# Kernel tuning notes

Hardware: AMD Instinct MI355X
Metric: run time of the kernel (lower is better)

## Reference

```python
import jax, jax.numpy as jnp
import numpy as np

D_IN = 1024
D_OUT = 1024
NUM_HEADS = 16
HEAD_DIM = D_OUT // NUM_HEADS


def setup_inputs() -> dict:
    key = jax.random.key(0)
    ks = jax.random.split(key, 6)
    scale = 0.02
    x = jax.random.normal(ks[0], (4, 2048, D_IN), dtype=jnp.float32)
    Wq = jax.random.normal(ks[1], (D_IN, D_OUT), dtype=jnp.float32) * scale
    Wk = jax.random.normal(ks[2], (D_IN, D_OUT), dtype=jnp.float32) * scale
    Wv = jax.random.normal(ks[3], (D_IN, D_OUT), dtype=jnp.float32) * scale
    Wo = jax.random.normal(ks[4], (D_OUT, D_OUT), dtype=jnp.float32) * scale
    bo = jax.random.normal(ks[5], (D_OUT,), dtype=jnp.float32) * scale
    return {"x": x, "Wq": Wq, "Wk": Wk, "Wv": Wv, "Wo": Wo, "bo": bo}


def reference(x, Wq, Wk, Wv, Wo, bo):
    b, n, _ = x.shape
    # QKV projections -> [b, h, n, hd]
    def split_heads(t):
        return t.reshape(b, n, NUM_HEADS, HEAD_DIM).transpose(0, 2, 1, 3)
    q = split_heads(x @ Wq)
    k = split_heads(x @ Wk)
    v = split_heads(x @ Wv)
    # scaled causal attention scores [b, h, n, n]
    scores = jnp.einsum('bhqd,bhkd->bhqk', q, k) / jnp.sqrt(jnp.float32(HEAD_DIM))
    causal = jnp.tril(jnp.ones((n, n), dtype=bool))
    scores = jnp.where(causal, scores, -jnp.inf)
    attn = jax.nn.softmax(scores, axis=-1)
    # dropout p=0.0 -> identity
    ctx = jnp.einsum('bhqk,bhkd->bhqd', attn, v)  # [b, h, n, hd]
    ctx = ctx.transpose(0, 2, 1, 3).reshape(b, n, D_OUT)
    return ctx @ Wo + bo
```

## Files before the change

### kernel.cpp

```cpp
#include <hip/hip_runtime.h>
#include <hip/hip_bf16.h>

typedef __bf16 bf16;
typedef __attribute__((ext_vector_type(8))) __bf16 bf16x8;
typedef __attribute__((ext_vector_type(4))) __bf16 bf16x4;
typedef __attribute__((ext_vector_type(4))) float floatx4;

#define DM 1024
#define NH 16
#define HD 64
#define SEQ 2048
#define BATCH 4
#define MTOT (BATCH * SEQ)

#define GLDS(g, l) \
  __builtin_amdgcn_global_load_lds((const __attribute__((address_space(1))) void*)(g), \
                                   (__attribute__((address_space(3))) void*)(l), 16, 0, 0)

__global__ void cvt_f32_bf16(const float* __restrict__ in, bf16* __restrict__ out, int n4) {
  int i = blockIdx.x * 256 + threadIdx.x;
  if (i < n4) {
    float4 v = ((const float4*)in)[i];
    bf16x4 o;
    o[0] = (bf16)v.x; o[1] = (bf16)v.y; o[2] = (bf16)v.z; o[3] = (bf16)v.w;
    ((bf16x4*)out)[i] = o;
  }
}

__global__ void transpose_cvt4(const float* __restrict__ Wq, const float* __restrict__ Wk,
                               const float* __restrict__ Wv, const float* __restrict__ Wo,
                               bf16* __restrict__ Wqkvt, bf16* __restrict__ Wot) {
  __shared__ float tile[32][33];
  const float* W;
  bf16* Wt;
  int z = blockIdx.z;
  if (z == 0) { W = Wq; Wt = Wqkvt; }
  else if (z == 1) { W = Wk; Wt = Wqkvt + (size_t)DM * DM; }
  else if (z == 2) { W = Wv; Wt = Wqkvt + (size_t)2 * DM * DM; }
  else { W = Wo; Wt = Wot; }
  int n0 = blockIdx.x * 32, k0 = blockIdx.y * 32;
  int tx = threadIdx.x, ty = threadIdx.y;
#pragma unroll
  for (int j = 0; j < 32; j += 8)
    tile[ty + j][tx] = W[(size_t)(k0 + ty + j) * DM + n0 + tx];
  __syncthreads();
#pragma unroll
  for (int j = 0; j < 32; j += 8)
    Wt[(size_t)(n0 + ty + j) * DM + k0 + tx] = (bf16)tile[tx][ty + j];
}

#define BK 64

__global__ __launch_bounds__(256, 3) void gemm_qkv(const bf16* __restrict__ A,
                                                   const bf16* __restrict__ Bt,
                                                   bf16* __restrict__ Qb,
                                                   bf16* __restrict__ Kb,
                                                   bf16* __restrict__ Vt) {
  __shared__ __align__(16) bf16 Alds[128 * BK];
  __shared__ __align__(16) bf16 Blds[128 * BK];
  const int K = 1024;
  int m0 = blockIdx.x * 128;
  int n0 = blockIdx.y * 128;
  int tid = threadIdx.x;
  int wave = tid >> 6, lane = tid & 63;
  int wm = (wave & 1) * 64, wn = (wave >> 1) * 64;
  int lm = lane & 15, quad = lane >> 4;
  int lm7 = lm & 7;

  int cbase = wave * 64 + lane;
  const bf16* gA[4];
  const bf16* gB[4];
  bf16 *lA[4], *lB[4];
#pragma unroll
  for (int seg = 0; seg < 4; ++seg) {
    int c = seg * 256 + cbase;
    int row = c >> 3;
    int col8 = (c & 7) ^ (row & 7);
    gA[seg] = A + (size_t)(m0 + row) * K + col8 * 8;
    gB[seg] = Bt + (size_t)(n0 + row) * K + col8 * 8;
    lA[seg] = Alds + c * 8;
    lB[seg] = Blds + c * 8;
  }

  floatx4 acc[4][4] = {};
  for (int kt = 0; kt < K; kt += BK) {
    __syncthreads();
#pragma unroll
    for (int seg = 0; seg < 4; ++seg) {
      GLDS(gA[seg] + kt, lA[seg]);
      GLDS(gB[seg] + kt, lB[seg]);
    }
    __syncthreads();
#pragma unroll
    for (int ks = 0; ks < 2; ++ks) {
      int xk = (ks * 4 + quad) ^ lm7;
      bf16x8 af[4], bfr[4];
#pragma unroll
      for (int t = 0; t < 4; ++t) {
        af[t] = *(const bf16x8*)(Alds + (wm + t * 16 + lm) * BK + xk * 8);
        bfr[t] = *(const bf16x8*)(Blds + (wn + t * 16 + lm) * BK + xk * 8);
      }
#pragma unroll
      for (int i = 0; i < 4; ++i)
#pragma unroll
        for (int j = 0; j < 4; ++j)
          acc[i][j] = __builtin_amdgcn_mfma_f32_16x16x32_bf16(af[i], bfr[j], acc[i][j], 0, 0, 0);
    }
  }
#pragma unroll
  for (int i = 0; i < 4; ++i) {
#pragma unroll
    for (int j = 0; j < 4; ++j) {
#pragma unroll
      for (int r = 0; r < 4; ++r) {
        int R = m0 + wm + i * 16 + quad * 4 + r;
        int C = n0 + wn + j * 16 + lm;
        int b = R >> 11, n = R & 2047;
        int proj = C >> 10, c = C & 1023;
        int h = c >> 6, d = c & 63;
        int bh = b * NH + h;
        bf16 bv = (bf16)acc[i][j][r];
        if (proj == 0)
          Qb[((size_t)bh * SEQ + n) * HD + d] = bv;
        else if (proj == 1)
          Kb[((size_t)bh * SEQ + n) * HD + d] = bv;
        else
          Vt[((size_t)bh * HD + d) * SEQ + n] = bv;
      }
    }
  }
}

__global__ __launch_bounds__(256, 3) void gemm_out(const bf16* __restrict__ A,
                                                   const bf16* __restrict__ Bt,
                                                   const float* __restrict__ bias,
                                                   float* __restrict__ out) {
  __shared__ __align__(16) bf16 Alds[128 * BK];
  __shared__ __align__(16) bf16 Blds[128 * BK];
  const int K = 1024;
  int m0 = blockIdx.x * 128;
  int n0 = blockIdx.y * 128;
  int tid = threadIdx.x;
  int wave = tid >> 6, lane = tid & 63;
  int wm = (wave & 1) * 64, wn = (wave >> 1) * 64;
  int lm = lane & 15, quad = lane >> 4;
  int lm7 = lm & 7;

  int cbase = wave * 64 + lane;
  const bf16* gA[4];
  const bf16* gB[4];
  bf16 *lA[4], *lB[4];
#pragma unroll
  for (int seg = 0; seg < 4; ++seg) {
    int c = seg * 256 + cbase;
    int row = c >> 3;
    int col8 = (c & 7) ^ (row & 7);
    gA[seg] = A + (size_t)(m0 + row) * K + col8 * 8;
    gB[seg] = Bt + (size_t)(n0 + row) * K + col8 * 8;
    lA[seg] = Alds + c * 8;
    lB[seg] = Blds + c * 8;
  }

  floatx4 acc[4][4] = {};
  for (int kt = 0; kt < K; kt += BK) {
    __syncthreads();
#pragma unroll
    for (int seg = 0; seg < 4; ++seg) {
      GLDS(gA[seg] + kt, lA[seg]);
      GLDS(gB[seg] + kt, lB[seg]);
    }
    __syncthreads();
#pragma unroll
    for (int ks = 0; ks < 2; ++ks) {
      int xk = (ks * 4 + quad) ^ lm7;
      bf16x8 af[4], bfr[4];
#pragma unroll
      for (int t = 0; t < 4; ++t) {
        af[t] = *(const bf16x8*)(Alds + (wm + t * 16 + lm) * BK + xk * 8);
        bfr[t] = *(const bf16x8*)(Blds + (wn + t * 16 + lm) * BK + xk * 8);
      }
#pragma unroll
      for (int i = 0; i < 4; ++i)
#pragma unroll
        for (int j = 0; j < 4; ++j)
          acc[i][j] = __builtin_amdgcn_mfma_f32_16x16x32_bf16(af[i], bfr[j], acc[i][j], 0, 0, 0);
    }
  }
#pragma unroll
  for (int i = 0; i < 4; ++i)
#pragma unroll
    for (int j = 0; j < 4; ++j)
#pragma unroll
      for (int r = 0; r < 4; ++r) {
        int R = m0 + wm + i * 16 + quad * 4 + r;
        int C = n0 + wn + j * 16 + lm;
        out[(size_t)R * DM + C] = acc[i][j][r] + bias[C];
      }
}

#define SKV 72

__global__ __launch_bounds__(256) void attn(const bf16* __restrict__ Qb,
                                            const bf16* __restrict__ Kb,
                                            const bf16* __restrict__ Vt,
                                            bf16* __restrict__ ctx) {
  __shared__ __align__(16) bf16 Klds[64 * SKV];
  __shared__ __align__(16) bf16 Vlds[64 * SKV];
  __shared__ __align__(16) bf16 Plds[4 * 16 * SKV];
  int blk = blockIdx.x;
  int xcd = blk & 7;
  int k = blk >> 3;
  int p = k & 15;
  int bh = (k >> 4) * 8 + xcd;
  int tid = threadIdx.x, wave = tid >> 6, lane = tid & 63;
  int lm = lane & 15, quad = lane >> 4;
  const bf16* Qp = Qb + (size_t)bh * SEQ * HD;
  const bf16* Kp = Kb + (size_t)bh * SEQ * HD;
  const bf16* Vp = Vt + (size_t)bh * HD * SEQ;
  bf16* Pl = Plds + wave * 16 * SKV;
  int sr = tid >> 3, sc = (tid & 7) * 8;
  int b = bh >> 4, h = bh & 15;

#pragma unroll 1
  for (int phase = 0; phase < 2; ++phase) {
    int qt = phase ? (31 - p) : p;
    int q0 = qt * 64;
    int rowbase = q0 + wave * 16;

    bf16x8 qf[2];
#pragma unroll
    for (int ks = 0; ks < 2; ++ks) {
      bf16x8 q = *(const bf16x8*)(Qp + (size_t)(rowbase + lm) * HD + ks * 32 + quad * 8);
#pragma unroll
      for (int j = 0; j < 8; ++j) q[j] = (bf16)((float)q[j] * 0.125f);
      qf[ks] = q;
    }

    floatx4 acco[4] = {};
    float lsum[4] = {};
    int nkv = qt + 1;

    bf16x8 ka0 = *(const bf16x8*)(Kp + (size_t)sr * HD + sc);
    bf16x8 ka1 = *(const bf16x8*)(Kp + (size_t)(32 + sr) * HD + sc);
    bf16x8 va0 = *(const bf16x8*)(Vp + (size_t)sr * SEQ + sc);
    bf16x8 va1 = *(const bf16x8*)(Vp + (size_t)(32 + sr) * SEQ + sc);
    __syncthreads();
    *(bf16x8*)(Klds + sr * SKV + sc) = ka0;
    *(bf16x8*)(Klds + (32 + sr) * SKV + sc) = ka1;
    *(bf16x8*)(Vlds + sr * SKV + sc) = va0;
    *(bf16x8*)(Vlds + (32 + sr) * SKV + sc) = va1;

#pragma unroll 1
    for (int t = 0; t < nkv; ++t) {
      __syncthreads();
      int kv0 = t * 64;
      if (t + 1 < nkv) {
        int kn = kv0 + 64;
        ka0 = *(const bf16x8*)(Kp + (size_t)(kn + sr) * HD + sc);
        ka1 = *(const bf16x8*)(Kp + (size_t)(kn + 32 + sr) * HD + sc);
        va0 = *(const bf16x8*)(Vp + (size_t)sr * SEQ + kn + sc);
        va1 = *(const bf16x8*)(Vp + (size_t)(32 + sr) * SEQ + kn + sc);
      }

      floatx4 s[4] = {};
#pragma unroll
      for (int nt = 0; nt < 4; ++nt) {
        bf16x8 kf0 = *(const bf16x8*)(Klds + (nt * 16 + lm) * SKV + quad * 8);
        bf16x8 kf1 = *(const bf16x8*)(Klds + (nt * 16 + lm) * SKV + 32 + quad * 8);
        s[nt] = __builtin_amdgcn_mfma_f32_16x16x32_bf16(qf[0], kf0, s[nt], 0, 0, 0);
        s[nt] = __builtin_amdgcn_mfma_f32_16x16x32_bf16(qf[1], kf1, s[nt], 0, 0, 0);
      }

      if (t != qt) {
#pragma unroll
        for (int nt = 0; nt < 4; ++nt)
#pragma unroll
          for (int r = 0; r < 4; ++r) {
            float pv = __expf(s[nt][r]);
            lsum[r] += pv;
            Pl[(quad * 4 + r) * SKV + nt * 16 + lm] = (bf16)pv;
          }
      } else {
#pragma unroll
        for (int nt = 0; nt < 4; ++nt)
#pragma unroll
          for (int r = 0; r < 4; ++r) {
            int rowrel = wave * 16 + quad * 4 + r;
            float pv = __expf(s[nt][r]);
            if (nt * 16 + lm > rowrel) pv = 0.f;
            lsum[r] += pv;
            Pl[(quad * 4 + r) * SKV + nt * 16 + lm] = (bf16)pv;
          }
      }

#pragma unroll
      for (int ks = 0; ks < 2; ++ks) {
        bf16x8 pf = *(const bf16x8*)(Pl + lm * SKV + ks * 32 + quad * 8);
#pragma unroll
        for (int db = 0; db < 4; ++db) {
          bf16x8 vf = *(const bf16x8*)(Vlds + (db * 16 + lm) * SKV + ks * 32 + quad * 8);
          acco[db] = __builtin_amdgcn_mfma_f32_16x16x32_bf16(pf, vf, acco[db], 0, 0, 0);
        }
      }

      if (t + 1 < nkv) {
        __syncthreads();
        *(bf16x8*)(Klds + sr * SKV + sc) = ka0;
        *(bf16x8*)(Klds + (32 + sr) * SKV + sc) = ka1;
        *(bf16x8*)(Vlds + sr * SKV + sc) = va0;
        *(bf16x8*)(Vlds + (32 + sr) * SKV + sc) = va1;
      }
    }

#pragma unroll
    for (int r = 0; r < 4; ++r) {
      float l = lsum[r];
      l += __shfl_xor(l, 1, 64);
      l += __shfl_xor(l, 2, 64);
      l += __shfl_xor(l, 4, 64);
      l += __shfl_xor(l, 8, 64);
      lsum[r] = 1.0f / l;
    }

#pragma unroll
    for (int db = 0; db < 4; ++db)
#pragma unroll
      for (int r = 0; r < 4; ++r) {
        int n = rowbase + quad * 4 + r;
        int col = h * 64 + db * 16 + lm;
        ctx[((size_t)b * SEQ + n) * DM + col] = (bf16)(acco[db][r] * lsum[r]);
      }
  }
}

extern "C" void kernel_launch(void* const* d_in, const int* in_sizes, int n_in,
                              void* d_out, int out_size, void* d_ws, size_t ws_size,
                              hipStream_t stream) {
  const float* x = (const float*)d_in[0];
  const float* Wq = (const float*)d_in[1];
  const float* Wk = (const float*)d_in[2];
  const float* Wv = (const float*)d_in[3];
  const float* Wo = (const float*)d_in[4];
  const float* bo = (const float*)d_in[5];
  float* out = (float*)d_out;

  bf16* ws = (bf16*)d_ws;
  bf16* xb = ws;
  bf16* Wqkvt = xb + (size_t)MTOT * DM;
  bf16* Wot = Wqkvt + (size_t)3 * DM * DM;
  bf16* Qb = Wot + (size_t)DM * DM;
  bf16* Kb = Qb + (size_t)BATCH * NH * SEQ * HD;
  bf16* Vtb = Kb + (size_t)BATCH * NH * SEQ * HD;
  bf16* ctx = xb;

  cvt_f32_bf16<<<(MTOT * DM / 4 + 255) / 256, 256, 0, stream>>>(x, xb, MTOT * DM / 4);
  transpose_cvt4<<<dim3(32, 32, 4), dim3(32, 8), 0, stream>>>(Wq, Wk, Wv, Wo, Wqkvt, Wot);
  gemm_qkv<<<dim3(MTOT / 128, 3 * DM / 128), 256, 0, stream>>>(xb, Wqkvt, Qb, Kb, Vtb);
  attn<<<1024, 256, 0, stream>>>(Qb, Kb, Vtb, ctx);
  gemm_out<<<dim3(MTOT / 128, DM / 128), 256, 0, stream>>>(ctx, Wot, bo, out);
}
```

Measured before the change: 257.1 us.

## Compute transposed S so P stays in registers, drop P LDS round-trip

The QK^T MFMA now takes K as the A operand and Q as the B operand, producing S^T. Each lane then holds one query's scores across keys, which matches the B-operand layout of the PV MFMA, so P is packed from registers and no longer staged through shared memory. The row-sum reduction becomes two cross-quad shuffles, and the output is written as vectorized bf16x4 stores. In exchange, V fragments are assembled from two 4-element LDS reads instead of one 8-element read.

```diff
diff --git a/kernel.cpp b/kernel.cpp
--- a/kernel.cpp
+++ b/kernel.cpp
@@ -206,7 +206,6 @@
                                             bf16* __restrict__ ctx) {
   __shared__ __align__(16) bf16 Klds[64 * SKV];
   __shared__ __align__(16) bf16 Vlds[64 * SKV];
-  __shared__ __align__(16) bf16 Plds[4 * 16 * SKV];
   int blk = blockIdx.x;
   int xcd = blk & 7;
   int k = blk >> 3;
@@ -217,7 +216,6 @@
   const bf16* Qp = Qb + (size_t)bh * SEQ * HD;
   const bf16* Kp = Kb + (size_t)bh * SEQ * HD;
   const bf16* Vp = Vt + (size_t)bh * HD * SEQ;
-  bf16* Pl = Plds + wave * 16 * SKV;
   int sr = tid >> 3, sc = (tid & 7) * 8;
   int b = bh >> 4, h = bh & 15;
 
@@ -237,7 +235,7 @@
     }
 
     floatx4 acco[4] = {};
-    float lsum[4] = {};
+    float lsum = 0.f;
     int nkv = qt + 1;
 
     bf16x8 ka0 = *(const bf16x8*)(Kp + (size_t)sr * HD + sc);
@@ -262,44 +260,52 @@
         va1 = *(const bf16x8*)(Vp + (size_t)(32 + sr) * SEQ + kn + sc);
       }
 
-      floatx4 s[4] = {};
-#pragma unroll
-      for (int nt = 0; nt < 4; ++nt) {
-        bf16x8 kf0 = *(const bf16x8*)(Klds + (nt * 16 + lm) * SKV + quad * 8);
-        bf16x8 kf1 = *(const bf16x8*)(Klds + (nt * 16 + lm) * SKV + 32 + quad * 8);
-        s[nt] = __builtin_amdgcn_mfma_f32_16x16x32_bf16(qf[0], kf0, s[nt], 0, 0, 0);
-        s[nt] = __builtin_amdgcn_mfma_f32_16x16x32_bf16(qf[1], kf1, s[nt], 0, 0, 0);
-      }
-
+      floatx4 st[4] = {};
+#pragma unroll
+      for (int mt = 0; mt < 4; ++mt) {
+        bf16x8 kf0 = *(const bf16x8*)(Klds + (mt * 16 + lm) * SKV + quad * 8);
+        bf16x8 kf1 = *(const bf16x8*)(Klds + (mt * 16 + lm) * SKV + 32 + quad * 8);
+        st[mt] = __builtin_amdgcn_mfma_f32_16x16x32_bf16(kf0, qf[0], st[mt], 0, 0, 0);
+        st[mt] = __builtin_amdgcn_mfma_f32_16x16x32_bf16(kf1, qf[1], st[mt], 0, 0, 0);
+      }
+
+      bf16x4 pb[4];
       if (t != qt) {
 #pragma unroll
-        for (int nt = 0; nt < 4; ++nt)
+        for (int mt = 0; mt < 4; ++mt)
 #pragma unroll
           for (int r = 0; r < 4; ++r) {
-            float pv = __expf(s[nt][r]);
-            lsum[r] += pv;
-            Pl[(quad * 4 + r) * SKV + nt * 16 + lm] = (bf16)pv;
+            float pv = __expf(st[mt][r]);
+            lsum += pv;
+            pb[mt][r] = (bf16)pv;
           }
       } else {
-#pragma unroll
-        for (int nt = 0; nt < 4; ++nt)
+        int qrel = wave * 16 + lm;
+#pragma unroll
+        for (int mt = 0; mt < 4; ++mt)
 #pragma unroll
           for (int r = 0; r < 4; ++r) {
-            int rowrel = wave * 16 + quad * 4 + r;
-            float pv = __expf(s[nt][r]);
-            if (nt * 16 + lm > rowrel) pv = 0.f;
-            lsum[r] += pv;
-            Pl[(quad * 4 + r) * SKV + nt * 16 + lm] = (bf16)pv;
+            float pv = __expf(st[mt][r]);
+            if (mt * 16 + quad * 4 + r > qrel) pv = 0.f;
+            lsum += pv;
+            pb[mt][r] = (bf16)pv;
           }
       }
 
 #pragma unroll
       for (int ks = 0; ks < 2; ++ks) {
-        bf16x8 pf = *(const bf16x8*)(Pl + lm * SKV + ks * 32 + quad * 8);
+        bf16x8 pf;
+#pragma unroll
+        for (int j = 0; j < 4; ++j) { pf[j] = pb[2 * ks][j]; pf[4 + j] = pb[2 * ks + 1][j]; }
 #pragma unroll
         for (int db = 0; db < 4; ++db) {
-          bf16x8 vf = *(const bf16x8*)(Vlds + (db * 16 + lm) * SKV + ks * 32 + quad * 8);
-          acco[db] = __builtin_amdgcn_mfma_f32_16x16x32_bf16(pf, vf, acco[db], 0, 0, 0);
+          const bf16* vrow = Vlds + (db * 16 + lm) * SKV + ks * 32 + quad * 4;
+          bf16x4 v0 = *(const bf16x4*)(vrow);
+          bf16x4 v1 = *(const bf16x4*)(vrow + 16);
+          bf16x8 vf;
+#pragma unroll
+          for (int j = 0; j < 4; ++j) { vf[j] = v0[j]; vf[4 + j] = v1[j]; }
+          acco[db] = __builtin_amdgcn_mfma_f32_16x16x32_bf16(vf, pf, acco[db], 0, 0, 0);
         }
       }
 
@@ -312,24 +318,18 @@
       }
     }
 
-#pragma unroll
-    for (int r = 0; r < 4; ++r) {
-      float l = lsum[r];
-      l += __shfl_xor(l, 1, 64);
-      l += __shfl_xor(l, 2, 64);
-      l += __shfl_xor(l, 4, 64);
-      l += __shfl_xor(l, 8, 64);
-      lsum[r] = 1.0f / l;
-    }
-
-#pragma unroll
-    for (int db = 0; db < 4; ++db)
-#pragma unroll
-      for (int r = 0; r < 4; ++r) {
-        int n = rowbase + quad * 4 + r;
-        int col = h * 64 + db * 16 + lm;
-        ctx[((size_t)b * SEQ + n) * DM + col] = (bf16)(acco[db][r] * lsum[r]);
-      }
+    lsum += __shfl_xor(lsum, 16, 64);
+    lsum += __shfl_xor(lsum, 32, 64);
+    float linv = 1.0f / lsum;
+
+    bf16* crow = ctx + ((size_t)b * SEQ + rowbase + lm) * DM + h * 64;
+#pragma unroll
+    for (int db = 0; db < 4; ++db) {
+      bf16x4 o;
+#pragma unroll
+      for (int r = 0; r < 4; ++r) o[r] = (bf16)(acco[db][r] * linv);
+      *(bf16x4*)(crow + db * 16 + quad * 4) = o;
+    }
   }
 }
 
```

New measurement: 255.6 us. No clear change (-0.6%).
